# Optimization experiments

Measured on AMD Instinct MI355X. Metric: run time of the kernel, lower is better.

The kernel has to match this reference:

```python
import jax, jax.numpy as jnp
import numpy as np

RETRIEVE_TEMP = 1.0
USAGE_SCALE = 0.5
CONF_SCALE = 0.5
SIG_SCALE = 1.0


def _l2norm(x, axis=-1, eps=1e-12):
    # matches torch F.normalize: x / max(||x||, eps)
    n = jnp.sqrt(jnp.sum(x * x, axis=axis, keepdims=True))
    return x / jnp.maximum(n, eps)


def setup_inputs() -> dict:
    key = jax.random.key(0)
    ks = jax.random.split(key, 7)
    N, T, U, B, S, R = 4, 2048, 64, 64, 128, 256
    q_u = jax.random.uniform(ks[0], (N, T, U), dtype=jnp.float32)
    q_b = jax.random.uniform(ks[1], (N, T, B), dtype=jnp.float32)
    q_sigma = jax.random.normal(ks[2], (N, T, S), dtype=jnp.float32)
    delta_rule_proto = jax.random.normal(ks[3], (U, B, R), dtype=jnp.float32)
    signature_proto = jax.random.normal(ks[4], (U, B, S), dtype=jnp.float32)
    # ~half of the cells have zero write mass so the validity mask is exercised
    write_mass = jnp.maximum(jax.random.uniform(ks[5], (U, B), dtype=jnp.float32) * 2.0 - 1.0, 0.0)
    ema_conf = jax.random.uniform(ks[6], (U, B), dtype=jnp.float32)
    return {"q_u": q_u, "q_b": q_b, "q_sigma": q_sigma,
            "delta_rule_proto": delta_rule_proto, "signature_proto": signature_proto,
            "write_mass": write_mass, "ema_conf": ema_conf}


def reference(q_u, q_b, q_sigma, delta_rule_proto, signature_proto, write_mass, ema_conf):
    # joint prob over (operator u, binding v): [n,t,u,v]
    joint = q_u[..., :, None] * q_b[..., None, :]
    valid = (write_mass > 0).astype(joint.dtype)            # [u,v]
    joint_logit = jnp.log(jnp.maximum(joint, 1e-6))

    usage_prior = jnp.log1p(write_mass)
    usage_prior = usage_prior / jnp.maximum(usage_prior.max(), 1.0)
    conf_prior = ema_conf / jnp.maximum(ema_conf.max(), 1e-6)

    qs = _l2norm(q_sigma)
    sp = _l2norm(signature_proto + 1e-6)
    sig_score = jnp.einsum('nts,uvs->ntuv', qs, sp)
    sig_score = 0.5 * (1.0 + sig_score)

    logits = (joint_logit + USAGE_SCALE * usage_prior + CONF_SCALE * conf_prior
              + SIG_SCALE * sig_score)                       # [n,t,u,v]

    batch_shape = logits.shape[:-2]
    UV = logits.shape[-2] * logits.shape[-1]
    flat_logits = logits.reshape(*batch_shape, UV)
    flat_valid = valid.reshape(UV)
    masked = jnp.where(flat_valid > 0, flat_logits, jnp.float32(-1e9))
    w = jax.nn.softmax(masked / RETRIEVE_TEMP, axis=-1)
    w = w * flat_valid
    w = w / jnp.maximum(jnp.sum(w, axis=-1, keepdims=True), 1e-6)  # [n,t,UV]

    weights = w.reshape(logits.shape)                        # [n,t,u,v]
    memory_delta_rule = jnp.einsum('ntuv,uvr->ntr', weights, delta_rule_proto)
    memory_signature = jnp.einsum('ntuv,uvs->nts', weights, signature_proto)

    flat_sig = sig_score.reshape(*batch_shape, UV)
    flat_conf = conf_prior.reshape(UV)
    top_index = jnp.argmax(w, axis=-1)                       # [n,t]
    top_weight = jnp.take_along_axis(w, top_index[..., None], axis=-1)
    top_conf = flat_conf[top_index][..., None]
    top_sig = jnp.take_along_axis(flat_sig, top_index[..., None], axis=-1)
    memory_conf = jnp.clip(top_weight * top_conf * top_sig, 0.0, 1.0)

    return (memory_delta_rule, memory_signature, memory_conf, weights, top_weight)
```

## Files before the change

### kernel.cpp

```cpp
#include <hip/hip_runtime.h>
#include <math.h>

#define NT   8192
#define UV   4096
#define SDIM 128
#define LOG1EM6 -13.815510557964274f

#define O_DELTA 0
#define O_SIG   2097152
#define O_CONF  3145728
#define O_W     3153920
#define O_TOPW  36708352

#define W_K4P   0
#define W_QSHI  0
#define W_QSLO  524288
#define W_SPHI  1048576
#define W_SPLO  1310720
#define W_LQU   1572864
#define W_LQB   2097152
#define W_BIAS  2621440
#define W_CONFN 2625536
#define W_VALID 2629632
#define W_PSUM  2633728
#define W_PMAX  2895872
#define W_PSIG  3158016
#define W_PUV   3420160
#define W_RINV  3682304
#define W_PTHI  3690496
#define W_PTLO  4476928

typedef __attribute__((ext_vector_type(8))) short short8;
typedef __attribute__((ext_vector_type(4))) float floatx4;

__device__ __forceinline__ unsigned short f2bf(float x) {
    unsigned u = __builtin_bit_cast(unsigned, x);
    u = u + 0x7fffu + ((u >> 16) & 1u);
    return (unsigned short)(u >> 16);
}
__device__ __forceinline__ float bf2f(unsigned short h) {
    unsigned u = ((unsigned)h) << 16;
    return __builtin_bit_cast(float, u);
}

__device__ __forceinline__ void gload_lds16(const void* g, void* l) {
    __builtin_amdgcn_global_load_lds(
        (const __attribute__((address_space(1))) unsigned*)g,
        (__attribute__((address_space(3))) unsigned*)l, 16, 0, 0);
}

__global__ void k1_tables(const float* __restrict__ wm,
                          const float* __restrict__ ec,
                          float* __restrict__ ws)
{
    __shared__ float red1[256];
    __shared__ float red2[256];
    const int tid = threadIdx.x;
    float m1 = 0.0f, m2 = 0.0f;
    for (int i = tid; i < UV; i += 256) {
        m1 = fmaxf(m1, log1pf(wm[i]));
        m2 = fmaxf(m2, ec[i]);
    }
    red1[tid] = m1; red2[tid] = m2;
    __syncthreads();
    for (int s = 128; s > 0; s >>= 1) {
        if (tid < s) {
            red1[tid] = fmaxf(red1[tid], red1[tid + s]);
            red2[tid] = fmaxf(red2[tid], red2[tid + s]);
        }
        __syncthreads();
    }
    const float inv1 = 1.0f / fmaxf(red1[0], 1.0f);
    const float inv2 = 1.0f / fmaxf(red2[0], 1e-6f);
    for (int i = tid; i < UV; i += 256) {
        float w  = wm[i];
        float un = log1pf(w) * inv1;
        float cn = ec[i] * inv2;
        ws[W_BIAS  + i] = 0.5f * un + 0.5f * cn;
        ws[W_CONFN + i] = cn;
        ws[W_VALID + i] = (w > 0.0f) ? 1.0f : 0.0f;
    }
}

__global__ void k2_norm(const float* __restrict__ spr,
                        const float* __restrict__ qsig,
                        float* __restrict__ ws)
{
    const int wid  = blockIdx.x * 4 + (threadIdx.x >> 6);
    const int lane = threadIdx.x & 63;
    if (wid < UV) {
        const float* src = spr + (size_t)wid * SDIM;
        float a = src[lane] + 1e-6f;
        float b = src[lane + 64] + 1e-6f;
        float ss = a * a + b * b;
        for (int m = 32; m > 0; m >>= 1) ss += __shfl_xor(ss, m);
        float inv = 1.0f / fmaxf(sqrtf(ss), 1e-12f);
        a *= inv; b *= inv;
        unsigned short* hi = (unsigned short*)(ws + W_SPHI);
        unsigned short* lo = (unsigned short*)(ws + W_SPLO);
        unsigned short ha = f2bf(a), hb = f2bf(b);
        hi[wid * 128 + lane]      = ha;
        hi[wid * 128 + lane + 64] = hb;
        lo[wid * 128 + lane]      = f2bf(a - bf2f(ha));
        lo[wid * 128 + lane + 64] = f2bf(b - bf2f(hb));
    } else {
        const int row = wid - UV;
        const float* src = qsig + (size_t)row * SDIM;
        float a = src[lane];
        float b = src[lane + 64];
        float ss = a * a + b * b;
        for (int m = 32; m > 0; m >>= 1) ss += __shfl_xor(ss, m);
        float inv = 1.0f / fmaxf(sqrtf(ss), 1e-12f);
        a *= inv; b *= inv;
        unsigned short* hi = (unsigned short*)(ws + W_QSHI);
        unsigned short* lo = (unsigned short*)(ws + W_QSLO);
        unsigned short ha = f2bf(a), hb = f2bf(b);
        hi[row * 128 + lane]      = ha;
        hi[row * 128 + lane + 64] = hb;
        lo[row * 128 + lane]      = f2bf(a - bf2f(ha));
        lo[row * 128 + lane + 64] = f2bf(b - bf2f(hb));
    }
}

__global__ __launch_bounds__(256)
void k2b_protoT(const float* __restrict__ drp, const float* __restrict__ spr,
                float* __restrict__ ws)
{
    __shared__ float tile[32][33];
    const int tid = threadIdx.x;
    const int k0 = blockIdx.x * 32;
    const int n0 = blockIdx.y * 32;
    {
        const int kr = tid >> 3, nc = (tid & 7) * 4;
        const int n = n0 + nc;
        float4 v;
        if (n < 256) v = *(const float4*)&drp[(size_t)(k0 + kr) * 256 + n];
        else         v = *(const float4*)&spr[(size_t)(k0 + kr) * 128 + (n - 256)];
        tile[kr][nc] = v.x; tile[kr][nc + 1] = v.y;
        tile[kr][nc + 2] = v.z; tile[kr][nc + 3] = v.w;
    }
    __syncthreads();
    {
        const int nr = tid >> 3, kc = (tid & 7) * 4;
        unsigned short* pth = (unsigned short*)(ws + W_PTHI);
        unsigned short* ptl = (unsigned short*)(ws + W_PTLO);
        ushort4 h, l;
        float x;
        x = tile[kc + 0][nr]; h.x = f2bf(x); l.x = f2bf(x - bf2f(h.x));
        x = tile[kc + 1][nr]; h.y = f2bf(x); l.y = f2bf(x - bf2f(h.y));
        x = tile[kc + 2][nr]; h.z = f2bf(x); l.z = f2bf(x - bf2f(h.z));
        x = tile[kc + 3][nr]; h.w = f2bf(x); l.w = f2bf(x - bf2f(h.w));
        *(ushort4*)&pth[(size_t)(n0 + nr) * 4096 + k0 + kc] = h;
        *(ushort4*)&ptl[(size_t)(n0 + nr) * 4096 + k0 + kc] = l;
    }
}

__global__ __launch_bounds__(256)
void k2c_logs(const float* __restrict__ qu, const float* __restrict__ qb,
              float* __restrict__ ws)
{
    const int t = blockIdx.x * 256 + threadIdx.x;
    const float* src = blockIdx.y ? qb : qu;
    float* dst = ws + (blockIdx.y ? W_LQB : W_LQU);
    float4 v = *(const float4*)&src[t * 4];
    v.x = __logf(v.x); v.y = __logf(v.y);
    v.z = __logf(v.z); v.w = __logf(v.w);
    *(float4*)&dst[t * 4] = v;
}

#define SA3 40

__global__ __launch_bounds__(256, 4)
void k3_mfma(float* __restrict__ ws, float* __restrict__ dout)
{
    __shared__ unsigned short sAh[64 * SA3];
    __shared__ unsigned short sAl[64 * SA3];
    __shared__ unsigned short sBh[128 * SA3];
    __shared__ unsigned short sBl[128 * SA3];
    __shared__ float sS[2][64], sM[2][64], sG[2][64], sU[2][64];

    const int tid  = threadIdx.x;
    const int row0 = blockIdx.x * 64;
    const int cb   = blockIdx.y;
    const int n0   = cb * 128;

    const unsigned short* qsh = (const unsigned short*)(ws + W_QSHI);
    const unsigned short* qsl = (const unsigned short*)(ws + W_QSLO);
    const unsigned short* sph = (const unsigned short*)(ws + W_SPHI);
    const unsigned short* spl = (const unsigned short*)(ws + W_SPLO);

    const int tAr = tid >> 2;
    const int tAk = (tid & 3) * 8;
    const int tBn = tid >> 2;
    const int tBk = (tid & 3) * 8;

    uint4 pah, pal, pbh[2], pbl[2];
    {
        pah = *(const uint4*)&qsh[(size_t)(row0 + tAr) * 128 + tAk];
        pal = *(const uint4*)&qsl[(size_t)(row0 + tAr) * 128 + tAk];
        #pragma unroll
        for (int p = 0; p < 2; ++p) {
            pbh[p] = *(const uint4*)&sph[(size_t)(n0 + tBn + p * 64) * 128 + tBk];
            pbl[p] = *(const uint4*)&spl[(size_t)(n0 + tBn + p * 64) * 128 + tBk];
        }
    }

    const int lane = tid & 63;
    const int wid  = tid >> 6;
    const int wm   = wid & 1;
    const int wn   = wid >> 1;
    const int fr   = lane & 15;
    const int fq   = lane >> 4;
    const int ako  = fq * 8;

    floatx4 acc[2][4];
    #pragma unroll
    for (int mt = 0; mt < 2; ++mt)
        #pragma unroll
        for (int nt = 0; nt < 4; ++nt)
            acc[mt][nt] = (floatx4){0.f, 0.f, 0.f, 0.f};

    for (int kc = 0; kc < 4; ++kc) {
        __syncthreads();
        *(uint4*)&sAh[tAr * SA3 + tAk] = pah;
        *(uint4*)&sAl[tAr * SA3 + tAk] = pal;
        #pragma unroll
        for (int p = 0; p < 2; ++p) {
            *(uint4*)&sBh[(tBn + p * 64) * SA3 + tBk] = pbh[p];
            *(uint4*)&sBl[(tBn + p * 64) * SA3 + tBk] = pbl[p];
        }
        __syncthreads();

        if (kc < 3) {
            const int kn = (kc + 1) * 32;
            pah = *(const uint4*)&qsh[(size_t)(row0 + tAr) * 128 + kn + tAk];
            pal = *(const uint4*)&qsl[(size_t)(row0 + tAr) * 128 + kn + tAk];
            #pragma unroll
            for (int p = 0; p < 2; ++p) {
                pbh[p] = *(const uint4*)&sph[(size_t)(n0 + tBn + p * 64) * 128 + kn + tBk];
                pbl[p] = *(const uint4*)&spl[(size_t)(n0 + tBn + p * 64) * 128 + kn + tBk];
            }
        }

        short8 afh[2], afl[2], bfh[4], bfl[4];
        #pragma unroll
        for (int mt = 0; mt < 2; ++mt) {
            const int m = wm * 32 + mt * 16 + fr;
            afh[mt] = *(const short8*)&sAh[m * SA3 + ako];
            afl[mt] = *(const short8*)&sAl[m * SA3 + ako];
        }
        #pragma unroll
        for (int nt = 0; nt < 4; ++nt) {
            const int n = wn * 64 + nt * 16 + fr;
            bfh[nt] = *(const short8*)&sBh[n * SA3 + ako];
            bfl[nt] = *(const short8*)&sBl[n * SA3 + ako];
        }
        #pragma unroll
        for (int mt = 0; mt < 2; ++mt)
            #pragma unroll
            for (int nt = 0; nt < 4; ++nt)
                acc[mt][nt] = __builtin_amdgcn_mfma_f32_16x16x32_bf16(
                    afh[mt], bfh[nt], acc[mt][nt], 0, 0, 0);
        #pragma unroll
        for (int mt = 0; mt < 2; ++mt)
            #pragma unroll
            for (int nt = 0; nt < 4; ++nt)
                acc[mt][nt] = __builtin_amdgcn_mfma_f32_16x16x32_bf16(
                    afh[mt], bfl[nt], acc[mt][nt], 0, 0, 0);
        #pragma unroll
        for (int mt = 0; mt < 2; ++mt)
            #pragma unroll
            for (int nt = 0; nt < 4; ++nt)
                acc[mt][nt] = __builtin_amdgcn_mfma_f32_16x16x32_bf16(
                    afl[mt], bfh[nt], acc[mt][nt], 0, 0, 0);
    }

    const float* lqu    = ws + W_LQU;
    const float* lqb    = ws + W_LQB;
    const float* bias   = ws + W_BIAS;
    const float* validf = ws + W_VALID;
    float* wout = dout + O_W;

    float ps[2][4], pm[2][4], pg[2][4], pu[2][4];
    #pragma unroll
    for (int mt = 0; mt < 2; ++mt)
        #pragma unroll
        for (int r = 0; r < 4; ++r) {
            ps[mt][r] = 0.f; pm[mt][r] = -1e30f; pg[mt][r] = 0.f; pu[mt][r] = 0.f;
        }

    #pragma unroll
    for (int mt = 0; mt < 2; ++mt) {
        const int rbase = row0 + wm * 32 + mt * 16 + fq * 4;
        #pragma unroll
        for (int nt = 0; nt < 4; ++nt) {
            const int uvb = n0 + wn * 64 + nt * 16;
            const int u   = uvb >> 6;
            const int uv  = uvb + fr;
            const int v   = uv & 63;
            const float bv = bias[uv];
            const float vd = validf[uv];
            const floatx4 a = acc[mt][nt];
            #pragma unroll
            for (int reg = 0; reg < 4; ++reg) {
                const int row = rbase + reg;
                const float jl  = fmaxf(lqu[(row << 6) + u] + lqb[(row << 6) + v], LOG1EM6);
                const float sig = fmaf(0.5f, a[reg], 0.5f);
                const float lg  = jl + bv + sig;
                const float e   = (vd > 0.f) ? __expf(lg - 2.f) : 0.f;
                wout[((size_t)row << 12) + uv] = e;
                ps[mt][reg] += e;
                if (vd > 0.f && lg > pm[mt][reg]) {
                    pm[mt][reg] = lg; pu[mt][reg] = (float)uv; pg[mt][reg] = sig;
                }
            }
        }
    }

    #pragma unroll
    for (int off = 1; off < 16; off <<= 1) {
        #pragma unroll
        for (int mt = 0; mt < 2; ++mt)
            #pragma unroll
            for (int r = 0; r < 4; ++r) {
                ps[mt][r] += __shfl_xor(ps[mt][r], off);
                float om = __shfl_xor(pm[mt][r], off);
                float ou = __shfl_xor(pu[mt][r], off);
                float og = __shfl_xor(pg[mt][r], off);
                if (om > pm[mt][r] || (om == pm[mt][r] && ou < pu[mt][r])) {
                    pm[mt][r] = om; pu[mt][r] = ou; pg[mt][r] = og;
                }
            }
    }
    if (fr == 0) {
        #pragma unroll
        for (int mt = 0; mt < 2; ++mt)
            #pragma unroll
            for (int r = 0; r < 4; ++r) {
                const int rl = wm * 32 + mt * 16 + fq * 4 + r;
                sS[wn][rl] = ps[mt][r]; sM[wn][rl] = pm[mt][r];
                sG[wn][rl] = pg[mt][r]; sU[wn][rl] = pu[mt][r];
            }
    }
    __syncthreads();
    if (tid < 64) {
        const float s  = sS[0][tid] + sS[1][tid];
        const float m0 = sM[0][tid], m1 = sM[1][tid];
        float m, uvf, g;
        if (m0 > m1 || (m0 == m1 && sU[0][tid] <= sU[1][tid])) {
            m = m0; uvf = sU[0][tid]; g = sG[0][tid];
        } else {
            m = m1; uvf = sU[1][tid]; g = sG[1][tid];
        }
        const int row = row0 + tid;
        ws[W_PSUM + cb * NT + row] = s;
        ws[W_PMAX + cb * NT + row] = m;
        ws[W_PSIG + cb * NT + row] = g;
        ws[W_PUV  + cb * NT + row] = uvf;
    }
}

__global__ __launch_bounds__(256)
void k3b_stats(float* __restrict__ ws, float* __restrict__ dout)
{
    const int row = blockIdx.x * 256 + threadIdx.x;
    float s = 0.f, m = -1e30f, uvf = 0.f, g = 0.f;
    for (int cb = 0; cb < 32; ++cb) {
        s += ws[W_PSUM + cb * NT + row];
        const float om = ws[W_PMAX + cb * NT + row];
        const float ou = ws[W_PUV  + cb * NT + row];
        const float og = ws[W_PSIG + cb * NT + row];
        if (om > m || (om == m && ou < uvf)) { m = om; uvf = ou; g = og; }
    }
    const float inv = 1.0f / s;
    ws[W_RINV + row] = inv;
    const float topw = __expf(m - 2.f) * inv;
    dout[O_TOPW + row] = topw;
    const int uvi = (int)uvf;
    const float cf = topw * ws[W_CONFN + uvi] * g;
    dout[O_CONF + row] = fminf(fmaxf(cf, 0.f), 1.f);
}

__global__ __launch_bounds__(256)
void k3c_scale(const float* __restrict__ ws, float* __restrict__ dout)
{
    float4* wb = (float4*)(dout + O_W);
    const float* rinv = ws + W_RINV;
    const int t = blockIdx.x * 256 + threadIdx.x;
    #pragma unroll 4
    for (int i = 0; i < 16; ++i) {
        const int idx = t + i * 524288;
        const float r = rinv[idx >> 10];
        float4 v = wb[idx];
        v.x *= r; v.y *= r; v.z *= r; v.w *= r;
        wb[idx] = v;
    }
}

__global__ __launch_bounds__(512, 2)
void k4_mfma(float* __restrict__ ws, float* __restrict__ dout)
{
    __shared__ unsigned short sB[2][2][192 * 32];

    const int tid  = threadIdx.x;
    const int lane = tid & 63;
    const int wv   = tid >> 6;

    const int bid   = blockIdx.x;
    const int xcd   = bid & 7;
    const int panel = xcd >> 1;
    const int ct    = panel & 1;
    const int ks    = panel >> 1;
    const int rt    = (bid >> 3) | ((xcd & 1) << 5);

    const int row0 = rt * 128;
    const int n0g  = ct * 192;
    const int kb   = ks * 2048;

    const float* wsrc = dout + O_W;
    const unsigned short* pth = (const unsigned short*)(ws + W_PTHI);
    const unsigned short* ptl = (const unsigned short*)(ws + W_PTLO);

    int st_pl[3], st_ldsoff[3], st_goff[3];
    #pragma unroll
    for (int j = 0; j < 3; ++j) {
        const int q   = wv * 3 + j;
        const int p   = (q >= 12) ? 1 : 0;
        const int qp  = q - p * 12;
        const int col = qp * 16 + (lane >> 2);
        const int s   = (lane & 3) ^ ((col >> 1) & 3);
        st_pl[j]     = p;
        st_ldsoff[j] = qp * 1024;
        st_goff[j]   = (n0g + col) * UV + s * 8;
    }

    const int fr = lane & 15;
    const int fq = lane >> 4;

    const float* aptr = wsrc + (size_t)(row0 + wv * 16 + fr) * UV + kb + fq * 8;

    int boff[12];
    #pragma unroll
    for (int nt = 0; nt < 12; ++nt) {
        const int col = nt * 16 + fr;
        boff[nt] = col * 32 + ((fq ^ ((col >> 1) & 3)) * 8);
    }

    floatx4 acc[12];
    #pragma unroll
    for (int nt = 0; nt < 12; ++nt)
        acc[nt] = (floatx4){0.f, 0.f, 0.f, 0.f};

    auto stage = [&](int kc_, int buf_) {
        const int kk = kb + kc_ * 32;
        #pragma unroll
        for (int j = 0; j < 3; ++j) {
            const unsigned short* src = (st_pl[j] ? ptl : pth) + st_goff[j] + kk;
            char* dst = (char*)(&sB[buf_][0][0]) + st_pl[j] * 12288 + st_ldsoff[j];
            gload_lds16(src, dst);
        }
    };

    stage(0, 0);
    float4 a0 = *(const float4*)(aptr);
    float4 a1 = *(const float4*)(aptr + 4);
    __syncthreads();

    int buf = 0;
    for (int kc = 0; kc < 64; ++kc) {
        float4 n0 = {}, n1 = {};
        if (kc + 1 < 64) {
            stage(kc + 1, buf ^ 1);
            n0 = *(const float4*)(aptr + (size_t)(kc + 1) * 32);
            n1 = *(const float4*)(aptr + (size_t)(kc + 1) * 32 + 4);
        }

        short8 afh, afl;
        {
            const float f[8] = {a0.x, a0.y, a0.z, a0.w, a1.x, a1.y, a1.z, a1.w};
            #pragma unroll
            for (int j = 0; j < 8; ++j) {
                const unsigned short h = f2bf(f[j]);
                afh[j] = (short)h;
                afl[j] = (short)f2bf(f[j] - bf2f(h));
            }
        }

        const unsigned short* bh = &sB[buf][0][0];
        const unsigned short* bl = &sB[buf][1][0];
        #pragma unroll
        for (int nt = 0; nt < 12; ++nt) {
            const short8 bfh = *(const short8*)&bh[boff[nt]];
            const short8 bfl = *(const short8*)&bl[boff[nt]];
            acc[nt] = __builtin_amdgcn_mfma_f32_16x16x32_bf16(afh, bfh, acc[nt], 0, 0, 0);
            acc[nt] = __builtin_amdgcn_mfma_f32_16x16x32_bf16(afh, bfl, acc[nt], 0, 0, 0);
            acc[nt] = __builtin_amdgcn_mfma_f32_16x16x32_bf16(afl, bfh, acc[nt], 0, 0, 0);
        }

        __syncthreads();
        a0 = n0; a1 = n1;
        buf ^= 1;
    }

    const int gr = row0 + wv * 16 + fq * 4;
    #pragma unroll
    for (int nt = 0; nt < 12; ++nt) {
        const int gc = n0g + nt * 16 + fr;
        const floatx4 a = acc[nt];
        if (ks == 0) {
            if (gc < 256) {
                float* o = dout + O_DELTA;
                o[(size_t)(gr + 0) * 256 + gc] = a[0];
                o[(size_t)(gr + 1) * 256 + gc] = a[1];
                o[(size_t)(gr + 2) * 256 + gc] = a[2];
                o[(size_t)(gr + 3) * 256 + gc] = a[3];
            } else {
                float* o = dout + O_SIG;
                const int c = gc - 256;
                o[(size_t)(gr + 0) * 128 + c] = a[0];
                o[(size_t)(gr + 1) * 128 + c] = a[1];
                o[(size_t)(gr + 2) * 128 + c] = a[2];
                o[(size_t)(gr + 3) * 128 + c] = a[3];
            }
        } else {
            float* p = ws + W_K4P;
            p[(size_t)(gr + 0) * 384 + gc] = a[0];
            p[(size_t)(gr + 1) * 384 + gc] = a[1];
            p[(size_t)(gr + 2) * 384 + gc] = a[2];
            p[(size_t)(gr + 3) * 384 + gc] = a[3];
        }
    }
}

__global__ __launch_bounds__(256)
void k4b_reduce(const float* __restrict__ ws, float* __restrict__ dout)
{
    const int idx = blockIdx.x * 256 + threadIdx.x;
    const int row = idx / 96;
    const int c   = (idx - row * 96) * 4;
    const float4 p = *(const float4*)&ws[W_K4P + (size_t)row * 384 + c];
    float* dst = (c < 256) ? (dout + O_DELTA + (size_t)row * 256 + c)
                           : (dout + O_SIG   + (size_t)row * 128 + (c - 256));
    float4 d = *(float4*)dst;
    d.x += p.x; d.y += p.y; d.z += p.z; d.w += p.w;
    *(float4*)dst = d;
}

extern "C" void kernel_launch(void* const* d_in, const int* in_sizes, int n_in,
                              void* d_out, int out_size, void* d_ws, size_t ws_size,
                              hipStream_t stream)
{
    const float* qu   = (const float*)d_in[0];
    const float* qb   = (const float*)d_in[1];
    const float* qsig = (const float*)d_in[2];
    const float* drp  = (const float*)d_in[3];
    const float* spr  = (const float*)d_in[4];
    const float* wm   = (const float*)d_in[5];
    const float* ec   = (const float*)d_in[6];
    float* out = (float*)d_out;
    float* ws  = (float*)d_ws;

    k1_tables<<<1, 256, 0, stream>>>(wm, ec, ws);
    k2_norm<<<3072, 256, 0, stream>>>(spr, qsig, ws);
    k2b_protoT<<<dim3(128, 12), 256, 0, stream>>>(drp, spr, ws);
    k2c_logs<<<dim3(512, 2), 256, 0, stream>>>(qu, qb, ws);
    k3_mfma<<<dim3(128, 32), 256, 0, stream>>>(ws, out);
    k3b_stats<<<32, 256, 0, stream>>>(ws, out);
    k3c_scale<<<2048, 256, 0, stream>>>(ws, out);
    k4_mfma<<<256, 512, 0, stream>>>(ws, out);
    k4b_reduce<<<3072, 256, 0, stream>>>(ws, out);
}
```

Baseline: 433.5 us.

## Merge prep kernels and fold softmax normalization into weighted-sum GEMM

Four small preprocessing kernels are merged into one launch that dispatches on block index. The separate pass that rescales the 128 MB weights tensor by the inverse row sum is removed. k4 now scales the unnormalized weights as it streams them and writes them back, and applies the inverse sum to its accumulators before storing. k4 is retiled to 64-row blocks in which each block covers all 384 output columns, so every weight row is read once per K-split and the write-back is done only by the wn==0 waves. This removes one full read and write of the weights tensor. In exchange there is a larger LDS staging footprint, launch bounds drop to one block per SM, and the unnormalized weights fed to the MFMA rely on rescaling later being exact enough.

```diff
diff --git a/kernel.cpp b/kernel.cpp
--- a/kernel.cpp
+++ b/kernel.cpp
@@ -49,123 +49,116 @@
         (__attribute__((address_space(3))) unsigned*)l, 16, 0, 0);
 }
 
-__global__ void k1_tables(const float* __restrict__ wm,
-                          const float* __restrict__ ec,
-                          float* __restrict__ ws)
+__global__ __launch_bounds__(256)
+void kprep(const float* __restrict__ qu, const float* __restrict__ qb,
+           const float* __restrict__ qsig, const float* __restrict__ drp,
+           const float* __restrict__ spr, const float* __restrict__ wm,
+           const float* __restrict__ ec, float* __restrict__ ws)
 {
     __shared__ float red1[256];
     __shared__ float red2[256];
+    __shared__ float tile[32][33];
+
+    const int bid = blockIdx.x;
     const int tid = threadIdx.x;
-    float m1 = 0.0f, m2 = 0.0f;
-    for (int i = tid; i < UV; i += 256) {
-        m1 = fmaxf(m1, log1pf(wm[i]));
-        m2 = fmaxf(m2, ec[i]);
-    }
-    red1[tid] = m1; red2[tid] = m2;
-    __syncthreads();
-    for (int s = 128; s > 0; s >>= 1) {
-        if (tid < s) {
-            red1[tid] = fmaxf(red1[tid], red1[tid + s]);
-            red2[tid] = fmaxf(red2[tid], red2[tid + s]);
+
+    if (bid < 3072) {
+        const int wid  = bid * 4 + (tid >> 6);
+        const int lane = tid & 63;
+        if (wid < UV) {
+            const float* src = spr + (size_t)wid * SDIM;
+            float a = src[lane] + 1e-6f;
+            float b = src[lane + 64] + 1e-6f;
+            float ss = a * a + b * b;
+            for (int m = 32; m > 0; m >>= 1) ss += __shfl_xor(ss, m);
+            float inv = 1.0f / fmaxf(sqrtf(ss), 1e-12f);
+            a *= inv; b *= inv;
+            unsigned short* hi = (unsigned short*)(ws + W_SPHI);
+            unsigned short* lo = (unsigned short*)(ws + W_SPLO);
+            unsigned short ha = f2bf(a), hb = f2bf(b);
+            hi[wid * 128 + lane]      = ha;
+            hi[wid * 128 + lane + 64] = hb;
+            lo[wid * 128 + lane]      = f2bf(a - bf2f(ha));
+            lo[wid * 128 + lane + 64] = f2bf(b - bf2f(hb));
+        } else {
+            const int row = wid - UV;
+            const float* src = qsig + (size_t)row * SDIM;
+            float a = src[lane];
+            float b = src[lane + 64];
+            float ss = a * a + b * b;
+            for (int m = 32; m > 0; m >>= 1) ss += __shfl_xor(ss, m);
+            float inv = 1.0f / fmaxf(sqrtf(ss), 1e-12f);
+            a *= inv; b *= inv;
+            unsigned short* hi = (unsigned short*)(ws + W_QSHI);
+            unsigned short* lo = (unsigned short*)(ws + W_QSLO);
+            unsigned short ha = f2bf(a), hb = f2bf(b);
+            hi[row * 128 + lane]      = ha;
+            hi[row * 128 + lane + 64] = hb;
+            lo[row * 128 + lane]      = f2bf(a - bf2f(ha));
+            lo[row * 128 + lane + 64] = f2bf(b - bf2f(hb));
+        }
+    } else if (bid < 4608) {
+        const int sub = bid - 3072;
+        const int k0  = (sub & 127) * 32;
+        const int n0  = (sub >> 7) * 32;
+        {
+            const int kr = tid >> 3, nc = (tid & 7) * 4;
+            const int n = n0 + nc;
+            float4 v;
+            if (n < 256) v = *(const float4*)&drp[(size_t)(k0 + kr) * 256 + n];
+            else         v = *(const float4*)&spr[(size_t)(k0 + kr) * 128 + (n - 256)];
+            tile[kr][nc] = v.x; tile[kr][nc + 1] = v.y;
+            tile[kr][nc + 2] = v.z; tile[kr][nc + 3] = v.w;
         }
         __syncthreads();
-    }
-    const float inv1 = 1.0f / fmaxf(red1[0], 1.0f);
-    const float inv2 = 1.0f / fmaxf(red2[0], 1e-6f);
-    for (int i = tid; i < UV; i += 256) {
-        float w  = wm[i];
-        float un = log1pf(w) * inv1;
-        float cn = ec[i] * inv2;
-        ws[W_BIAS  + i] = 0.5f * un + 0.5f * cn;
-        ws[W_CONFN + i] = cn;
-        ws[W_VALID + i] = (w > 0.0f) ? 1.0f : 0.0f;
-    }
-}
-
-__global__ void k2_norm(const float* __restrict__ spr,
-                        const float* __restrict__ qsig,
-                        float* __restrict__ ws)
-{
-    const int wid  = blockIdx.x * 4 + (threadIdx.x >> 6);
-    const int lane = threadIdx.x & 63;
-    if (wid < UV) {
-        const float* src = spr + (size_t)wid * SDIM;
-        float a = src[lane] + 1e-6f;
-        float b = src[lane + 64] + 1e-6f;
-        float ss = a * a + b * b;
-        for (int m = 32; m > 0; m >>= 1) ss += __shfl_xor(ss, m);
-        float inv = 1.0f / fmaxf(sqrtf(ss), 1e-12f);
-        a *= inv; b *= inv;
-        unsigned short* hi = (unsigned short*)(ws + W_SPHI);
-        unsigned short* lo = (unsigned short*)(ws + W_SPLO);
-        unsigned short ha = f2bf(a), hb = f2bf(b);
-        hi[wid * 128 + lane]      = ha;
-        hi[wid * 128 + lane + 64] = hb;
-        lo[wid * 128 + lane]      = f2bf(a - bf2f(ha));
-        lo[wid * 128 + lane + 64] = f2bf(b - bf2f(hb));
+        {
+            const int nr = tid >> 3, kc = (tid & 7) * 4;
+            unsigned short* pth = (unsigned short*)(ws + W_PTHI);
+            unsigned short* ptl = (unsigned short*)(ws + W_PTLO);
+            ushort4 h, l;
+            float x;
+            x = tile[kc + 0][nr]; h.x = f2bf(x); l.x = f2bf(x - bf2f(h.x));
+            x = tile[kc + 1][nr]; h.y = f2bf(x); l.y = f2bf(x - bf2f(h.y));
+            x = tile[kc + 2][nr]; h.z = f2bf(x); l.z = f2bf(x - bf2f(h.z));
+            x = tile[kc + 3][nr]; h.w = f2bf(x); l.w = f2bf(x - bf2f(h.w));
+            *(ushort4*)&pth[(size_t)(n0 + nr) * 4096 + k0 + kc] = h;
+            *(ushort4*)&ptl[(size_t)(n0 + nr) * 4096 + k0 + kc] = l;
+        }
+    } else if (bid < 5632) {
+        const int sub = bid - 4608;
+        const int t = (sub & 511) * 256 + tid;
+        const float* src = (sub >> 9) ? qb : qu;
+        float* dst = ws + ((sub >> 9) ? W_LQB : W_LQU);
+        float4 v = *(const float4*)&src[t * 4];
+        v.x = __logf(v.x); v.y = __logf(v.y);
+        v.z = __logf(v.z); v.w = __logf(v.w);
+        *(float4*)&dst[t * 4] = v;
     } else {
-        const int row = wid - UV;
-        const float* src = qsig + (size_t)row * SDIM;
-        float a = src[lane];
-        float b = src[lane + 64];
-        float ss = a * a + b * b;
-        for (int m = 32; m > 0; m >>= 1) ss += __shfl_xor(ss, m);
-        float inv = 1.0f / fmaxf(sqrtf(ss), 1e-12f);
-        a *= inv; b *= inv;
-        unsigned short* hi = (unsigned short*)(ws + W_QSHI);
-        unsigned short* lo = (unsigned short*)(ws + W_QSLO);
-        unsigned short ha = f2bf(a), hb = f2bf(b);
-        hi[row * 128 + lane]      = ha;
-        hi[row * 128 + lane + 64] = hb;
-        lo[row * 128 + lane]      = f2bf(a - bf2f(ha));
-        lo[row * 128 + lane + 64] = f2bf(b - bf2f(hb));
-    }
-}
-
-__global__ __launch_bounds__(256)
-void k2b_protoT(const float* __restrict__ drp, const float* __restrict__ spr,
-                float* __restrict__ ws)
-{
-    __shared__ float tile[32][33];
-    const int tid = threadIdx.x;
-    const int k0 = blockIdx.x * 32;
-    const int n0 = blockIdx.y * 32;
-    {
-        const int kr = tid >> 3, nc = (tid & 7) * 4;
-        const int n = n0 + nc;
-        float4 v;
-        if (n < 256) v = *(const float4*)&drp[(size_t)(k0 + kr) * 256 + n];
-        else         v = *(const float4*)&spr[(size_t)(k0 + kr) * 128 + (n - 256)];
-        tile[kr][nc] = v.x; tile[kr][nc + 1] = v.y;
-        tile[kr][nc + 2] = v.z; tile[kr][nc + 3] = v.w;
-    }
-    __syncthreads();
-    {
-        const int nr = tid >> 3, kc = (tid & 7) * 4;
-        unsigned short* pth = (unsigned short*)(ws + W_PTHI);
-        unsigned short* ptl = (unsigned short*)(ws + W_PTLO);
-        ushort4 h, l;
-        float x;
-        x = tile[kc + 0][nr]; h.x = f2bf(x); l.x = f2bf(x - bf2f(h.x));
-        x = tile[kc + 1][nr]; h.y = f2bf(x); l.y = f2bf(x - bf2f(h.y));
-        x = tile[kc + 2][nr]; h.z = f2bf(x); l.z = f2bf(x - bf2f(h.z));
-        x = tile[kc + 3][nr]; h.w = f2bf(x); l.w = f2bf(x - bf2f(h.w));
-        *(ushort4*)&pth[(size_t)(n0 + nr) * 4096 + k0 + kc] = h;
-        *(ushort4*)&ptl[(size_t)(n0 + nr) * 4096 + k0 + kc] = l;
-    }
-}
-
-__global__ __launch_bounds__(256)
-void k2c_logs(const float* __restrict__ qu, const float* __restrict__ qb,
-              float* __restrict__ ws)
-{
-    const int t = blockIdx.x * 256 + threadIdx.x;
-    const float* src = blockIdx.y ? qb : qu;
-    float* dst = ws + (blockIdx.y ? W_LQB : W_LQU);
-    float4 v = *(const float4*)&src[t * 4];
-    v.x = __logf(v.x); v.y = __logf(v.y);
-    v.z = __logf(v.z); v.w = __logf(v.w);
-    *(float4*)&dst[t * 4] = v;
+        float m1 = 0.0f, m2 = 0.0f;
+        for (int i = tid; i < UV; i += 256) {
+            m1 = fmaxf(m1, log1pf(wm[i]));
+            m2 = fmaxf(m2, ec[i]);
+        }
+        red1[tid] = m1; red2[tid] = m2;
+        __syncthreads();
+        for (int s = 128; s > 0; s >>= 1) {
+            if (tid < s) {
+                red1[tid] = fmaxf(red1[tid], red1[tid + s]);
+                red2[tid] = fmaxf(red2[tid], red2[tid + s]);
+            }
+            __syncthreads();
+        }
+        const float inv1 = 1.0f / fmaxf(red1[0], 1.0f);
+        const float inv2 = 1.0f / fmaxf(red2[0], 1e-6f);
+        for (int i = tid; i < UV; i += 256) {
+            float w  = wm[i];
+            float un = log1pf(w) * inv1;
+            float cn = ec[i] * inv2;
+            ws[W_BIAS  + i] = 0.5f * un + 0.5f * cn;
+            ws[W_CONFN + i] = cn;
+            ws[W_VALID + i] = (w > 0.0f) ? 1.0f : 0.0f;
+        }
+    }
 }
 
 #define SA3 40
@@ -381,68 +374,54 @@
     dout[O_CONF + row] = fminf(fmaxf(cf, 0.f), 1.f);
 }
 
-__global__ __launch_bounds__(256)
-void k3c_scale(const float* __restrict__ ws, float* __restrict__ dout)
-{
-    float4* wb = (float4*)(dout + O_W);
-    const float* rinv = ws + W_RINV;
-    const int t = blockIdx.x * 256 + threadIdx.x;
-    #pragma unroll 4
-    for (int i = 0; i < 16; ++i) {
-        const int idx = t + i * 524288;
-        const float r = rinv[idx >> 10];
-        float4 v = wb[idx];
-        v.x *= r; v.y *= r; v.z *= r; v.w *= r;
-        wb[idx] = v;
-    }
-}
-
-__global__ __launch_bounds__(512, 2)
+__global__ __launch_bounds__(512, 1)
 void k4_mfma(float* __restrict__ ws, float* __restrict__ dout)
 {
-    __shared__ unsigned short sB[2][2][192 * 32];
+    __shared__ unsigned short sB[2][2][12288];
 
     const int tid  = threadIdx.x;
     const int lane = tid & 63;
     const int wv   = tid >> 6;
 
-    const int bid   = blockIdx.x;
-    const int xcd   = bid & 7;
-    const int panel = xcd >> 1;
-    const int ct    = panel & 1;
-    const int ks    = panel >> 1;
-    const int rt    = (bid >> 3) | ((xcd & 1) << 5);
-
-    const int row0 = rt * 128;
-    const int n0g  = ct * 192;
+    const int bid = blockIdx.x;
+    const int xcd = bid & 7;
+    const int ks  = xcd >> 2;
+    const int rt  = ((bid >> 3) << 2) | (xcd & 3);
+    const int row0 = rt * 64;
     const int kb   = ks * 2048;
 
-    const float* wsrc = dout + O_W;
     const unsigned short* pth = (const unsigned short*)(ws + W_PTHI);
     const unsigned short* ptl = (const unsigned short*)(ws + W_PTLO);
 
-    int st_pl[3], st_ldsoff[3], st_goff[3];
-    #pragma unroll
-    for (int j = 0; j < 3; ++j) {
-        const int q   = wv * 3 + j;
-        const int p   = (q >= 12) ? 1 : 0;
-        const int qp  = q - p * 12;
-        const int col = qp * 16 + (lane >> 2);
-        const int s   = (lane & 3) ^ ((col >> 1) & 3);
-        st_pl[j]     = p;
-        st_ldsoff[j] = qp * 1024;
-        st_goff[j]   = (n0g + col) * UV + s * 8;
+    int st_pl[6], st_ubase[6], st_goff[6];
+    #pragma unroll
+    for (int j = 0; j < 6; ++j) {
+        const int cu = (tid & ~63) + j * 512;
+        const int c  = cu + lane;
+        const int pl = (cu >= 1536) ? 1 : 0;
+        const int cc = c - pl * 1536;
+        const int col = cc >> 2;
+        const int sl  = (cc & 3) ^ ((col >> 1) & 3);
+        st_pl[j]    = pl;
+        st_ubase[j] = pl * 24576 + (cu - pl * 1536) * 16;
+        st_goff[j]  = col * UV + sl * 8;
     }
 
     const int fr = lane & 15;
     const int fq = lane >> 4;
 
-    const float* aptr = wsrc + (size_t)(row0 + wv * 16 + fr) * UV + kb + fq * 8;
+    const int wm = wv & 3;
+    const int wn = wv >> 2;
+
+    const int arow = row0 + wm * 16 + fr;
+    const float* aptr = dout + O_W + (size_t)arow * UV + kb + fq * 8;
+    float*       awb  = dout + O_W + (size_t)arow * UV + kb + fq * 8;
+    const float rinv_a = ws[W_RINV + arow];
 
     int boff[12];
     #pragma unroll
     for (int nt = 0; nt < 12; ++nt) {
-        const int col = nt * 16 + fr;
+        const int col = wn * 192 + nt * 16 + fr;
         boff[nt] = col * 32 + ((fq ^ ((col >> 1) & 3)) * 8);
     }
 
@@ -454,9 +433,9 @@
     auto stage = [&](int kc_, int buf_) {
         const int kk = kb + kc_ * 32;
         #pragma unroll
-        for (int j = 0; j < 3; ++j) {
+        for (int j = 0; j < 6; ++j) {
             const unsigned short* src = (st_pl[j] ? ptl : pth) + st_goff[j] + kk;
-            char* dst = (char*)(&sB[buf_][0][0]) + st_pl[j] * 12288 + st_ldsoff[j];
+            char* dst = (char*)(&sB[buf_][0][0]) + st_ubase[j];
             gload_lds16(src, dst);
         }
     };
@@ -466,6 +445,7 @@
     float4 a1 = *(const float4*)(aptr + 4);
     __syncthreads();
 
+    float4 p0 = {}, p1 = {};
     int buf = 0;
     for (int kc = 0; kc < 64; ++kc) {
         float4 n0 = {}, n1 = {};
@@ -475,6 +455,16 @@
             n1 = *(const float4*)(aptr + (size_t)(kc + 1) * 32 + 4);
         }
 
+        if (wn == 0 && kc > 0) {
+            float4 w0, w1;
+            w0.x = p0.x * rinv_a; w0.y = p0.y * rinv_a;
+            w0.z = p0.z * rinv_a; w0.w = p0.w * rinv_a;
+            w1.x = p1.x * rinv_a; w1.y = p1.y * rinv_a;
+            w1.z = p1.z * rinv_a; w1.w = p1.w * rinv_a;
+            *(float4*)(awb + (size_t)(kc - 1) * 32)     = w0;
+            *(float4*)(awb + (size_t)(kc - 1) * 32 + 4) = w1;
+        }
+
         short8 afh, afl;
         {
             const float f[8] = {a0.x, a0.y, a0.z, a0.w, a1.x, a1.y, a1.z, a1.w};
@@ -497,16 +487,31 @@
             acc[nt] = __builtin_amdgcn_mfma_f32_16x16x32_bf16(afl, bfh, acc[nt], 0, 0, 0);
         }
 
+        p0 = a0; p1 = a1;
         __syncthreads();
         a0 = n0; a1 = n1;
         buf ^= 1;
     }
-
-    const int gr = row0 + wv * 16 + fq * 4;
+    if (wn == 0) {
+        float4 w0, w1;
+        w0.x = p0.x * rinv_a; w0.y = p0.y * rinv_a;
+        w0.z = p0.z * rinv_a; w0.w = p0.w * rinv_a;
+        w1.x = p1.x * rinv_a; w1.y = p1.y * rinv_a;
+        w1.z = p1.z * rinv_a; w1.w = p1.w * rinv_a;
+        *(float4*)(awb + (size_t)63 * 32)     = w0;
+        *(float4*)(awb + (size_t)63 * 32 + 4) = w1;
+    }
+
+    const int gr = row0 + wm * 16 + fq * 4;
+    float rv[4];
+    #pragma unroll
+    for (int r = 0; r < 4; ++r) rv[r] = ws[W_RINV + gr + r];
+
     #pragma unroll
     for (int nt = 0; nt < 12; ++nt) {
-        const int gc = n0g + nt * 16 + fr;
-        const floatx4 a = acc[nt];
+        const int gc = wn * 192 + nt * 16 + fr;
+        floatx4 a = acc[nt];
+        a[0] *= rv[0]; a[1] *= rv[1]; a[2] *= rv[2]; a[3] *= rv[3];
         if (ks == 0) {
             if (gc < 256) {
                 float* o = dout + O_DELTA;
@@ -560,13 +565,9 @@
     float* out = (float*)d_out;
     float* ws  = (float*)d_ws;
 
-    k1_tables<<<1, 256, 0, stream>>>(wm, ec, ws);
-    k2_norm<<<3072, 256, 0, stream>>>(spr, qsig, ws);
-    k2b_protoT<<<dim3(128, 12), 256, 0, stream>>>(drp, spr, ws);
-    k2c_logs<<<dim3(512, 2), 256, 0, stream>>>(qu, qb, ws);
+    kprep<<<5633, 256, 0, stream>>>(qu, qb, qsig, drp, spr, wm, ec, ws);
     k3_mfma<<<dim3(128, 32), 256, 0, stream>>>(ws, out);
     k3b_stats<<<32, 256, 0, stream>>>(ws, out);
-    k3c_scale<<<2048, 256, 0, stream>>>(ws, out);
     k4_mfma<<<256, 512, 0, stream>>>(ws, out);
     k4b_reduce<<<3072, 256, 0, stream>>>(ws, out);
 }
```

Measured after the change: 426.4 us. Within noise of the previous version (-1.6%).
